# Optimization experiments

Measured on AMD Instinct MI355X. Metric: run time of the kernel, lower is better.

The kernel has to match this reference:

```python
import jax, jax.numpy as jnp
import numpy as np

B, N, C = 8, 4096, 1024
H, D = 16, 64
FF = 4096
EPS_ATTN = 1e-6
EPS_LN = 1e-5


def layer_norm(x, g, b, eps=EPS_LN):
    mu = jnp.mean(x, axis=-1, keepdims=True)
    var = jnp.mean(jnp.square(x - mu), axis=-1, keepdims=True)
    return (x - mu) * jax.lax.rsqrt(var + eps) * g + b


def phi(x):
    # elu(x) + 1
    return jnp.where(x > 0, x + 1.0, jnp.exp(x))


def setup_inputs() -> dict:
    key = jax.random.key(0)
    ks = jax.random.split(key, 8)
    src = jax.random.normal(ks[0], (B, N, C), dtype=jnp.float32)
    lengths = jax.random.randint(ks[1], (B,), int(0.75 * N), N + 1)
    src_key_padding_mask = jnp.arange(N)[None, :] >= lengths[:, None]
    s = 0.02
    qkv_w = jax.random.normal(ks[2], (3 * C, C), dtype=jnp.float32) * s
    qkv_b = jnp.zeros((3 * C,), jnp.float32)
    out_w = jax.random.normal(ks[3], (C, C), dtype=jnp.float32) * s
    out_b = jnp.zeros((C,), jnp.float32)
    w1 = jax.random.normal(ks[4], (FF, C), dtype=jnp.float32) * s
    b1 = jnp.zeros((FF,), jnp.float32)
    w2 = jax.random.normal(ks[5], (C, FF), dtype=jnp.float32) * s
    b2 = jnp.zeros((C,), jnp.float32)
    ln1_g = jnp.ones((C,), jnp.float32)
    ln1_b = jnp.zeros((C,), jnp.float32)
    ln2_g = jnp.ones((C,), jnp.float32)
    ln2_b = jnp.zeros((C,), jnp.float32)
    return dict(src=src, src_key_padding_mask=src_key_padding_mask,
                qkv_w=qkv_w, qkv_b=qkv_b, out_w=out_w, out_b=out_b,
                w1=w1, b1=b1, w2=w2, b2=b2,
                ln1_g=ln1_g, ln1_b=ln1_b, ln2_g=ln2_g, ln2_b=ln2_b)


def linear_attention(x, mask, qkv_w, qkv_b, out_w, out_b):
    b, n, c = x.shape
    qkv = (x @ qkv_w.T + qkv_b).reshape(b, n, 3, H, D)
    qkv = jnp.transpose(qkv, (2, 0, 3, 1, 4))  # [3,B,H,N,D]
    q, k, v = qkv[0], qkv[1], qkv[2]
    qf, kf = phi(q), phi(k)
    valid = (~mask).astype(kf.dtype)[:, None, :, None]  # [B,1,N,1]
    kf = kf * valid
    v = v * valid
    kv = jnp.einsum('bhnd,bhne->bhde', kf, v)          # [B,H,D,D]
    z = kf.sum(axis=2)                                  # [B,H,D]
    y_num = jnp.einsum('bhnd,bhde->bhne', qf, kv)       # [B,H,N,D]
    y_den = jnp.maximum(jnp.einsum('bhnd,bhd->bhn', qf, z), EPS_ATTN)
    y = y_num / y_den[..., None]
    y = jnp.transpose(y, (0, 2, 1, 3)).reshape(b, n, c)
    return y @ out_w.T + out_b


def reference(src, src_key_padding_mask, qkv_w, qkv_b, out_w, out_b,
              w1, b1, w2, b2, ln1_g, ln1_b, ln2_g, ln2_b):
    # pre-norm: attention block
    attn_out = linear_attention(layer_norm(src, ln1_g, ln1_b), src_key_padding_mask,
                                qkv_w, qkv_b, out_w, out_b)
    x = src + attn_out
    # pre-norm: FFN block (exact gelu, matching torch F.gelu default)
    h = jax.nn.gelu(layer_norm(x, ln2_g, ln2_b) @ w1.T + b1, approximate=False)
    return x + (h @ w2.T + b2)
```

## Files before the change

### kernel.cpp

```cpp
#include <hip/hip_runtime.h>
#include <cmath>
#include <cstdint>

#define MTOK 32768
#define CDIM 1024
#define SEQ  4096
#define NHEAD 16
#define HDIM 64
#define FFDIM 4096

typedef __attribute__((ext_vector_type(8))) short short8;
typedef __attribute__((ext_vector_type(4))) float f32x4;

static __device__ __forceinline__ float b2f(unsigned short u){
  union { unsigned int i; float f; } c; c.i = ((unsigned int)u)<<16; return c.f;
}
static __device__ __forceinline__ unsigned short f2b(float f){
  union { float f; unsigned int i; } c; c.f = f;
  return (unsigned short)((c.i + 0x7fffu + ((c.i>>16)&1u)) >> 16);
}
static __device__ __forceinline__ void async16(const void* g, void* l){
  __builtin_amdgcn_global_load_lds((const __attribute__((address_space(1))) void*)g,
                                   (__attribute__((address_space(3))) void*)l, 16, 0, 0);
}

__global__ void detect_mask_kernel(const unsigned int* __restrict__ m, int* __restrict__ flag){
  __shared__ int any;
  if(threadIdx.x==0) any=0;
  __syncthreads();
  int loc=0;
  for(int i=threadIdx.x;i<8192;i+=256) if(m[i]>1u) loc=1;
  if(loc) atomicOr(&any,1);
  __syncthreads();
  if(threadIdx.x==0) *flag=any;
}
__global__ void decode_mask_kernel(const void* __restrict__ m, const int* __restrict__ flag,
                                   float* __restrict__ validf){
  int i = blockIdx.x*256 + threadIdx.x;
  int pad = (*flag) ? (int)((const unsigned char*)m)[i] : ((const int*)m)[i];
  validf[i] = pad ? 0.f : 1.f;
}

__global__ void cast_bf16_kernel(const float* __restrict__ x, unsigned short* __restrict__ y, int n){
  int i = (blockIdx.x*256 + threadIdx.x)*4;
  if(i>=n) return;
  float4 v = *(const float4*)(x+i);
  ushort4 o; o.x=f2b(v.x); o.y=f2b(v.y); o.z=f2b(v.z); o.w=f2b(v.w);
  *(ushort4*)(y+i)=o;
}

__global__ __launch_bounds__(256) void ln_kernel(const float* __restrict__ x,
    const float* __restrict__ g, const float* __restrict__ bt, unsigned short* __restrict__ out){
  int row = blockIdx.x, t = threadIdx.x;
  const float* xr = x + (size_t)row*CDIM;
  float4 v = *(const float4*)(xr + t*4);
  float s1 = v.x+v.y+v.z+v.w;
  float s2 = v.x*v.x+v.y*v.y+v.z*v.z+v.w*v.w;
  #pragma unroll
  for(int off=32; off>0; off>>=1){ s1+=__shfl_down(s1,off); s2+=__shfl_down(s2,off); }
  __shared__ float a1[4], a2[4];
  __shared__ float mu_s, rs_s;
  if((t&63)==0){ a1[t>>6]=s1; a2[t>>6]=s2; }
  __syncthreads();
  if(t==0){
    float u1=a1[0]+a1[1]+a1[2]+a1[3], u2=a2[0]+a2[1]+a2[2]+a2[3];
    float mu=u1*(1.f/CDIM);
    mu_s=mu; rs_s=rsqrtf(u2*(1.f/CDIM)-mu*mu+1e-5f);
  }
  __syncthreads();
  float mu=mu_s, rs=rs_s;
  float4 gg=*(const float4*)(g+t*4), bb=*(const float4*)(bt+t*4);
  ushort4 o;
  o.x=f2b((v.x-mu)*rs*gg.x+bb.x);
  o.y=f2b((v.y-mu)*rs*gg.y+bb.y);
  o.z=f2b((v.z-mu)*rs*gg.z+bb.z);
  o.w=f2b((v.w-mu)*rs*gg.w+bb.w);
  *(ushort4*)(out+(size_t)row*CDIM+t*4)=o;
}

template<int MODE>
__global__ __launch_bounds__(512,2) void gemm_bt(
    const unsigned short* __restrict__ A, const unsigned short* __restrict__ Bw,
    const float* __restrict__ bias, const float* __restrict__ extra,
    float* __restrict__ Cf, unsigned short* __restrict__ Cb,
    int M, int N, int K)
{
  __shared__ __align__(16) unsigned short As[2*2*128*64];
  __shared__ __align__(16) unsigned short Bs[2*2*128*64];
  const int tid  = threadIdx.x;
  const int lane = tid & 63, wave = tid >> 6;
  const int wm = wave >> 2, wn = wave & 3;
  const int gx  = gridDim.x;
  const int f   = blockIdx.y * gx + blockIdx.x;
  const int xcd = f & 7, kk = f >> 3;
  const int nx  = kk % gx;
  const int ny  = (kk / gx) * 8 + xcd;
  const int m0 = ny*256, n0 = nx*256;
  const int r8  = lane >> 3;
  const int gch = ((lane & 7) ^ r8) * 8;
  const int l15 = lane & 15;
  const int kc  = lane >> 4, x7 = lane & 7;
  const int ch0 = ( kc      ^ x7) * 8;
  const int ch1 = ((kc + 4) ^ x7) * 8;
  const int NT  = K >> 6;

  f32x4 acc[2][2][4][2];
  #pragma unroll
  for(int a0=0;a0<2;a0++)
    #pragma unroll
    for(int a1=0;a1<2;a1++)
      #pragma unroll
      for(int a2=0;a2<4;a2++)
        #pragma unroll
        for(int a3=0;a3<2;a3++) acc[a0][a1][a2][a3]=(f32x4)(0.f);

  auto stageA = [&](int h, int bb, int kcol){
    const unsigned short* g = A + (size_t)(m0 + h*128 + wave*8 + r8)*K + kcol + gch;
    unsigned short* l = &As[((bb*2 + h)*128 + wave*8)*64];
    async16(g, l);
    async16(g + (size_t)64*K, l + 64*64);
  };
  auto stageB = [&](int h, int bb, int kcol){
    const unsigned short* g = Bw + (size_t)(n0 + h*128 + wave*8 + r8)*K + kcol + gch;
    unsigned short* l = &Bs[((bb*2 + h)*128 + wave*8)*64];
    async16(g, l);
    async16(g + (size_t)64*K, l + 64*64);
  };

  #define READ_A(H,BB) { const unsigned short* Ab=&As[((BB)*2+(H))*128*64];         \
    _Pragma("unroll") for(int fi=0;fi<4;fi++){ int ro=(wm*64+fi*16+l15)*64;          \
      af[fi][0]=*(const short8*)&Ab[ro+ch0];                                         \
      af[fi][1]=*(const short8*)&Ab[ro+ch1]; } }
  #define READ_B(H,BB,DST) { const unsigned short* Bb=&Bs[((BB)*2+(H))*128*64];      \
    _Pragma("unroll") for(int ni=0;ni<2;ni++){ int ro=(wn*32+ni*16+l15)*64;          \
      DST[ni][0]=*(const short8*)&Bb[ro+ch0];                                        \
      DST[ni][1]=*(const short8*)&Bb[ro+ch1]; } }
  #define QUAD(MQ,NQ,BV) {                                                           \
    _Pragma("unroll") for(int fi=0;fi<4;fi++)                                        \
      _Pragma("unroll") for(int ni=0;ni<2;ni++){                                     \
        acc[MQ][NQ][fi][ni]=__builtin_amdgcn_mfma_f32_16x16x32_bf16(                 \
            af[fi][0],BV[ni][0],acc[MQ][NQ][fi][ni],0,0,0);                          \
        acc[MQ][NQ][fi][ni]=__builtin_amdgcn_mfma_f32_16x16x32_bf16(                 \
            af[fi][1],BV[ni][1],acc[MQ][NQ][fi][ni],0,0,0); } }

  stageA(0,0,0); stageA(1,0,0); stageB(0,0,0); stageB(1,0,0);
  if(NT>1){
    stageA(0,1,64); stageB(0,1,64);
    asm volatile("s_waitcnt vmcnt(4)" ::: "memory");
  } else {
    asm volatile("s_waitcnt vmcnt(0)" ::: "memory");
  }
  __builtin_amdgcn_s_barrier();

  for(int t=0; t<NT; ++t){
    const int bi = t & 1, bo = (t+1) & 1;
    const int k1 = (t+1) << 6, k2 = (t+2) << 6;
    short8 af[4][2], b0v[2][2], b1v[2][2];

    READ_A(0,bi); READ_B(0,bi,b0v);
    if(t+1<NT) stageA(1,bo,k1);
    __builtin_amdgcn_s_barrier();
    asm volatile("s_waitcnt lgkmcnt(0)" ::: "memory");
    __builtin_amdgcn_s_setprio(1); QUAD(0,0,b0v); __builtin_amdgcn_s_setprio(0);
    __builtin_amdgcn_s_barrier();

    READ_B(1,bi,b1v);
    if(t+1<NT) stageB(1,bo,k1);
    __builtin_amdgcn_s_barrier();
    asm volatile("s_waitcnt lgkmcnt(0)" ::: "memory");
    __builtin_amdgcn_s_setprio(1); QUAD(0,1,b1v); __builtin_amdgcn_s_setprio(0);
    __builtin_amdgcn_s_barrier();

    READ_A(1,bi);
    if(t+2<NT) stageA(0,bi,k2);
    __builtin_amdgcn_s_barrier();
    asm volatile("s_waitcnt lgkmcnt(0)" ::: "memory");
    __builtin_amdgcn_s_setprio(1); QUAD(1,0,b0v); __builtin_amdgcn_s_setprio(0);
    __builtin_amdgcn_s_barrier();

    if(t+2<NT) stageB(0,bi,k2);
    __builtin_amdgcn_s_barrier();
    asm volatile("s_waitcnt lgkmcnt(0)" ::: "memory");
    __builtin_amdgcn_s_setprio(1); QUAD(1,1,b1v); __builtin_amdgcn_s_setprio(0);
    if(t+2<NT){ asm volatile("s_waitcnt vmcnt(4)" ::: "memory"); }
    else      { asm volatile("s_waitcnt vmcnt(0)" ::: "memory"); }
    __builtin_amdgcn_s_barrier();
  }
  #undef READ_A
  #undef READ_B
  #undef QUAD

  const int rb0 = (lane>>4)*4;
  #pragma unroll
  for(int mq=0;mq<2;mq++){
    #pragma unroll
    for(int fi=0;fi<4;fi++){
      #pragma unroll
      for(int i=0;i<4;i++){
        int m = m0 + mq*128 + wm*64 + fi*16 + rb0 + i;
        float valid = (MODE==0) ? extra[m] : 0.f;
        #pragma unroll
        for(int nq=0;nq<2;nq++){
          #pragma unroll
          for(int ni=0;ni<2;ni++){
            int n = n0 + nq*128 + wn*32 + ni*16 + l15;
            float v = acc[mq][nq][fi][ni][i] + bias[n];
            if(MODE==0){
              int part = n>>10;
              float p = (v>0.f)? (v+1.f) : __expf(v);
              float r = (part==0)? p : (part==1? p*valid : v*valid);
              Cb[(size_t)m*N + n] = f2b(r);
            } else if(MODE==1){
              size_t off=(size_t)m*N+n;
              Cf[off] = v + extra[off];
            } else if(MODE==2){
              float gl = 0.5f*v*(1.f+erff(v*0.70710678118654752f));
              Cb[(size_t)m*N+n] = f2b(gl);
            } else {
              size_t off=(size_t)m*N+n;
              Cf[off] += v;
            }
          }
        }
      }
    }
  }
}

__global__ __launch_bounds__(256) void kvz_partial_kernel(
    const unsigned short* __restrict__ qkv, float* __restrict__ kvp, float* __restrict__ zp)
{
  const int chunk = blockIdx.x;
  const int bh = blockIdx.y;
  const int b = bh>>4, h = bh&15;
  const int t = threadIdx.x;
  __shared__ float kfs[16][64];
  __shared__ float vs[16][64];
  float acc[4][4]={{0}}; float zacc[4]={0};
  const int td=t&15, te=t>>4;
  const int d0=td*4, e0=te*4;
  const int lr=t>>4, lc=(t&15)*4;
  for(int s=0;s<16;s++){
    size_t m  = (size_t)(b*SEQ + chunk*256 + s*16 + lr);
    size_t rb = m*3072 + (size_t)h*64;
    ushort4 k4 = *(const ushort4*)(qkv + rb + 1024 + lc);
    ushort4 v4 = *(const ushort4*)(qkv + rb + 2048 + lc);
    __syncthreads();
    kfs[lr][lc]=b2f(k4.x); kfs[lr][lc+1]=b2f(k4.y); kfs[lr][lc+2]=b2f(k4.z); kfs[lr][lc+3]=b2f(k4.w);
    vs [lr][lc]=b2f(v4.x); vs [lr][lc+1]=b2f(v4.y); vs [lr][lc+2]=b2f(v4.z); vs [lr][lc+3]=b2f(v4.w);
    __syncthreads();
    #pragma unroll
    for(int n=0;n<16;n++){
      float4 kq=*(const float4*)&kfs[n][d0];
      float4 vv=*(const float4*)&vs[n][e0];
      float kqa[4]={kq.x,kq.y,kq.z,kq.w};
      float vva[4]={vv.x,vv.y,vv.z,vv.w};
      #pragma unroll
      for(int i=0;i<4;i++)
        #pragma unroll
        for(int j=0;j<4;j++) acc[i][j]+=kqa[i]*vva[j];
      if(te==0){ zacc[0]+=kq.x; zacc[1]+=kq.y; zacc[2]+=kq.z; zacc[3]+=kq.w; }
    }
  }
  const int pidx = bh*16 + chunk;
  float* kvd = kvp + (size_t)pidx*4096;
  #pragma unroll
  for(int i=0;i<4;i++){
    float4 o={acc[i][0],acc[i][1],acc[i][2],acc[i][3]};
    *(float4*)(kvd + (d0+i)*64 + e0)=o;
  }
  if(te==0){
    float4 o={zacc[0],zacc[1],zacc[2],zacc[3]};
    *(float4*)(zp + (size_t)pidx*64 + d0)=o;
  }
}

__global__ void kvz_reduce_kernel(const float* __restrict__ kvp, const float* __restrict__ zp,
                                  float* __restrict__ kv, float* __restrict__ z){
  int bh = blockIdx.x, t = threadIdx.x;
  for(int j=t; j<4096; j+=256){
    float s=0;
    for(int c=0;c<16;c++) s += kvp[((size_t)bh*16+c)*4096 + j];
    kv[(size_t)bh*4096 + j] = s;
  }
  if(t<64){
    float s=0;
    for(int c=0;c<16;c++) s += zp[((size_t)bh*16+c)*64 + t];
    z[bh*64+t]=s;
  }
}

__global__ __launch_bounds__(256) void y_kernel(
    const unsigned short* __restrict__ qkv, const float* __restrict__ kv,
    const float* __restrict__ z, unsigned short* __restrict__ ybuf)
{
  const int nch = blockIdx.x;
  const int bh  = blockIdx.y;
  const int b = bh>>4, h = bh&15;
  const int t = threadIdx.x;
  __shared__ float kvs[64][64];
  __shared__ float qfs[64][68];
  __shared__ float zs[64];
  for(int j=t*4; j<4096; j+=1024){
    float4 vv=*(const float4*)(kv+(size_t)bh*4096+j);
    ((float*)kvs)[j]=vv.x; ((float*)kvs)[j+1]=vv.y; ((float*)kvs)[j+2]=vv.z; ((float*)kvs)[j+3]=vv.w;
  }
  if(t<64) zs[t]=z[bh*64+t];
  for(int s=0;s<4;s++){
    int row=s*16+(t>>4), col=(t&15)*4;
    size_t m=(size_t)(b*SEQ+nch*64+row);
    ushort4 q4=*(const ushort4*)(qkv+m*3072+(size_t)h*64+col);
    qfs[row][col]=b2f(q4.x); qfs[row][col+1]=b2f(q4.y); qfs[row][col+2]=b2f(q4.z); qfs[row][col+3]=b2f(q4.w);
  }
  __syncthreads();
  const int tn=t>>4, te=t&15;
  const int nr0=tn*4, e0=te*4;
  float acc[4][4]={{0}}; float den[4]={0};
  #pragma unroll 4
  for(int d=0;d<64;d++){
    float4 kv4=*(const float4*)&kvs[d][e0];
    float zd=zs[d];
    #pragma unroll
    for(int i=0;i<4;i++){
      float q=qfs[nr0+i][d];
      acc[i][0]+=q*kv4.x; acc[i][1]+=q*kv4.y; acc[i][2]+=q*kv4.z; acc[i][3]+=q*kv4.w;
      den[i]+=q*zd;
    }
  }
  #pragma unroll
  for(int i=0;i<4;i++){
    float inv=1.f/fmaxf(den[i],1e-6f);
    ushort4 o;
    o.x=f2b(acc[i][0]*inv); o.y=f2b(acc[i][1]*inv); o.z=f2b(acc[i][2]*inv); o.w=f2b(acc[i][3]*inv);
    size_t m=(size_t)(b*SEQ+nch*64+nr0+i);
    *(ushort4*)(ybuf+m*1024+(size_t)h*64+e0)=o;
  }
}

extern "C" void kernel_launch(void* const* d_in, const int* in_sizes, int n_in,
                              void* d_out, int out_size, void* d_ws, size_t ws_size,
                              hipStream_t stream)
{
  const float* src   = (const float*)d_in[0];
  const void*  mask  = d_in[1];
  const float* qkv_w = (const float*)d_in[2];
  const float* qkv_b = (const float*)d_in[3];
  const float* out_w = (const float*)d_in[4];
  const float* out_b = (const float*)d_in[5];
  const float* w1    = (const float*)d_in[6];
  const float* b1    = (const float*)d_in[7];
  const float* w2    = (const float*)d_in[8];
  const float* b2    = (const float*)d_in[9];
  const float* ln1g  = (const float*)d_in[10];
  const float* ln1b  = (const float*)d_in[11];
  const float* ln2g  = (const float*)d_in[12];
  const float* ln2b  = (const float*)d_in[13];
  float* out = (float*)d_out;
  char* ws = (char*)d_ws;

  size_t o = 0;
  int* flag = (int*)(ws);                         o += 256;
  float* validf = (float*)(ws+o);                 o += (size_t)MTOK*4;
  unsigned short* wqb = (unsigned short*)(ws+o);  o += (size_t)3072*1024*2;
  unsigned short* wob = (unsigned short*)(ws+o);  o += (size_t)1024*1024*2;
  unsigned short* w1b = (unsigned short*)(ws+o);  o += (size_t)4096*1024*2;
  unsigned short* w2b = (unsigned short*)(ws+o);  o += (size_t)1024*4096*2;
  unsigned short* bufA = (unsigned short*)(ws+o); o += (size_t)MTOK*1024*2;
  char* R = ws+o;                                 o += (size_t)MTOK*4096*2;
  unsigned short* qkvbuf = (unsigned short*)R;
  float* kvp = (float*)(R + (size_t)MTOK*3072*2);
  float* zp  = (float*)(R + (size_t)MTOK*3072*2 + (size_t)2048*4096*4);
  unsigned short* hbuf = (unsigned short*)R;
  float* kv = (float*)(ws+o);                     o += (size_t)128*4096*4;
  float* zv = (float*)(ws+o);                     o += (size_t)128*64*4;

  detect_mask_kernel<<<1,256,0,stream>>>((const unsigned int*)mask, flag);
  decode_mask_kernel<<<MTOK/256,256,0,stream>>>(mask, flag, validf);
  cast_bf16_kernel<<<3072,256,0,stream>>>(qkv_w, wqb, 3072*1024);
  cast_bf16_kernel<<<1024,256,0,stream>>>(out_w, wob, 1024*1024);
  cast_bf16_kernel<<<4096,256,0,stream>>>(w1,  w1b, 4096*1024);
  cast_bf16_kernel<<<8192,256,0,stream>>>(w2,  w2b, 1024*4096);

  ln_kernel<<<MTOK,256,0,stream>>>(src, ln1g, ln1b, bufA);
  gemm_bt<0><<<dim3(3072/256, MTOK/256),512,0,stream>>>(bufA, wqb, qkv_b, validf, nullptr, qkvbuf, MTOK,3072,1024);
  kvz_partial_kernel<<<dim3(16,128),256,0,stream>>>(qkvbuf, kvp, zp);
  kvz_reduce_kernel<<<128,256,0,stream>>>(kvp, zp, kv, zv);
  y_kernel<<<dim3(64,128),256,0,stream>>>(qkvbuf, kv, zv, bufA);
  gemm_bt<1><<<dim3(1024/256, MTOK/256),512,0,stream>>>(bufA, wob, out_b, src, out, nullptr, MTOK,1024,1024);
  ln_kernel<<<MTOK,256,0,stream>>>(out, ln2g, ln2b, bufA);
  gemm_bt<2><<<dim3(4096/256, MTOK/256),512,0,stream>>>(bufA, w1b, b1, nullptr, nullptr, hbuf, MTOK,4096,1024);
  gemm_bt<3><<<dim3(1024/256, MTOK/256),512,0,stream>>>(hbuf, w2b, b2, nullptr, out, nullptr, MTOK,1024,4096);
}
```

Baseline: 1.561 ms.

## Template GEMM on K and reorder async LDS staging for deeper prefetch

Makes the K dimension a template parameter so address arithmetic and trip counts are compile-time constants, and precomputes per-thread global base pointers. Reorders the async global-to-LDS staging so three tiles are in flight at the prologue and next-tile loads are issued earlier within each iteration, with vmcnt waits raised to match. It also relaxes the lgkmcnt waits and adds a sched_barrier, aiming to hide global load latency behind MFMA work. The buffer reuse ordering changes, which risks races if the waits and barriers don't exactly cover overwritten LDS regions.

```diff
diff --git a/kernel.cpp b/kernel.cpp
--- a/kernel.cpp
+++ b/kernel.cpp
@@ -78,12 +78,12 @@
   *(ushort4*)(out+(size_t)row*CDIM+t*4)=o;
 }
 
-template<int MODE>
+template<int MODE, int KDIM>
 __global__ __launch_bounds__(512,2) void gemm_bt(
     const unsigned short* __restrict__ A, const unsigned short* __restrict__ Bw,
     const float* __restrict__ bias, const float* __restrict__ extra,
     float* __restrict__ Cf, unsigned short* __restrict__ Cb,
-    int M, int N, int K)
+    int M, int N)
 {
   __shared__ __align__(16) unsigned short As[2*2*128*64];
   __shared__ __align__(16) unsigned short Bs[2*2*128*64];
@@ -98,11 +98,13 @@
   const int m0 = ny*256, n0 = nx*256;
   const int r8  = lane >> 3;
   const int gch = ((lane & 7) ^ r8) * 8;
+  const unsigned short* gA = A  + (size_t)(m0 + wave*8 + r8)*KDIM + gch;
+  const unsigned short* gB = Bw + (size_t)(n0 + wave*8 + r8)*KDIM + gch;
   const int l15 = lane & 15;
   const int kc  = lane >> 4, x7 = lane & 7;
   const int ch0 = ( kc      ^ x7) * 8;
   const int ch1 = ((kc + 4) ^ x7) * 8;
-  const int NT  = K >> 6;
+  const int NT  = KDIM >> 6;
 
   f32x4 acc[2][2][4][2];
   #pragma unroll
@@ -114,17 +116,17 @@
         #pragma unroll
         for(int a3=0;a3<2;a3++) acc[a0][a1][a2][a3]=(f32x4)(0.f);
 
-  auto stageA = [&](int h, int bb, int kcol){
-    const unsigned short* g = A + (size_t)(m0 + h*128 + wave*8 + r8)*K + kcol + gch;
+  auto stA = [&](int h, int bb, int kcol){
+    const unsigned short* g = gA + (size_t)h*128*KDIM + kcol;
     unsigned short* l = &As[((bb*2 + h)*128 + wave*8)*64];
     async16(g, l);
-    async16(g + (size_t)64*K, l + 64*64);
+    async16(g + (size_t)64*KDIM, l + 4096);
   };
-  auto stageB = [&](int h, int bb, int kcol){
-    const unsigned short* g = Bw + (size_t)(n0 + h*128 + wave*8 + r8)*K + kcol + gch;
+  auto stB = [&](int h, int bb, int kcol){
+    const unsigned short* g = gB + (size_t)h*128*KDIM + kcol;
     unsigned short* l = &Bs[((bb*2 + h)*128 + wave*8)*64];
     async16(g, l);
-    async16(g + (size_t)64*K, l + 64*64);
+    async16(g + (size_t)64*KDIM, l + 4096);
   };
 
   #define READ_A(H,BB) { const unsigned short* Ab=&As[((BB)*2+(H))*128*64];         \
@@ -143,47 +145,48 @@
         acc[MQ][NQ][fi][ni]=__builtin_amdgcn_mfma_f32_16x16x32_bf16(                 \
             af[fi][1],BV[ni][1],acc[MQ][NQ][fi][ni],0,0,0); } }
 
-  stageA(0,0,0); stageA(1,0,0); stageB(0,0,0); stageB(1,0,0);
+  stA(0,0,0); stB(0,0,0); stB(1,0,0); stA(1,0,0);
   if(NT>1){
-    stageA(0,1,64); stageB(0,1,64);
-    asm volatile("s_waitcnt vmcnt(4)" ::: "memory");
+    stA(0,1,64); stB(0,1,64); stA(1,1,64);
+    asm volatile("s_waitcnt vmcnt(6)" ::: "memory");
   } else {
     asm volatile("s_waitcnt vmcnt(0)" ::: "memory");
   }
   __builtin_amdgcn_s_barrier();
 
   for(int t=0; t<NT; ++t){
-    const int bi = t & 1, bo = (t+1) & 1;
+    const int bi = t & 1, bo = bi ^ 1;
     const int k1 = (t+1) << 6, k2 = (t+2) << 6;
     short8 af[4][2], b0v[2][2], b1v[2][2];
 
     READ_A(0,bi); READ_B(0,bi,b0v);
-    if(t+1<NT) stageA(1,bo,k1);
-    __builtin_amdgcn_s_barrier();
-    asm volatile("s_waitcnt lgkmcnt(0)" ::: "memory");
+    if(t+1<NT) stB(1,bo,k1);
+    asm volatile("s_waitcnt lgkmcnt(8)");
+    __builtin_amdgcn_s_barrier();
+    asm volatile("s_waitcnt lgkmcnt(0)");
     __builtin_amdgcn_s_setprio(1); QUAD(0,0,b0v); __builtin_amdgcn_s_setprio(0);
     __builtin_amdgcn_s_barrier();
 
     READ_B(1,bi,b1v);
-    if(t+1<NT) stageB(1,bo,k1);
-    __builtin_amdgcn_s_barrier();
-    asm volatile("s_waitcnt lgkmcnt(0)" ::: "memory");
+    if(t+2<NT) stA(0,bi,k2);
+    __builtin_amdgcn_s_barrier();
+    asm volatile("s_waitcnt lgkmcnt(0)");
     __builtin_amdgcn_s_setprio(1); QUAD(0,1,b1v); __builtin_amdgcn_s_setprio(0);
     __builtin_amdgcn_s_barrier();
 
     READ_A(1,bi);
-    if(t+2<NT) stageA(0,bi,k2);
-    __builtin_amdgcn_s_barrier();
-    asm volatile("s_waitcnt lgkmcnt(0)" ::: "memory");
+    if(t+2<NT) stB(0,bi,k2);
+    __builtin_amdgcn_s_barrier();
+    asm volatile("s_waitcnt lgkmcnt(0)");
     __builtin_amdgcn_s_setprio(1); QUAD(1,0,b0v); __builtin_amdgcn_s_setprio(0);
     __builtin_amdgcn_s_barrier();
 
-    if(t+2<NT) stageB(0,bi,k2);
-    __builtin_amdgcn_s_barrier();
-    asm volatile("s_waitcnt lgkmcnt(0)" ::: "memory");
+    if(t+2<NT) stA(1,bi,k2);
+    __builtin_amdgcn_s_barrier();
     __builtin_amdgcn_s_setprio(1); QUAD(1,1,b1v); __builtin_amdgcn_s_setprio(0);
-    if(t+2<NT){ asm volatile("s_waitcnt vmcnt(4)" ::: "memory"); }
+    if(t+2<NT){ asm volatile("s_waitcnt vmcnt(6)" ::: "memory"); }
     else      { asm volatile("s_waitcnt vmcnt(0)" ::: "memory"); }
+    __builtin_amdgcn_sched_barrier(0);
     __builtin_amdgcn_s_barrier();
   }
   #undef READ_A
@@ -382,12 +385,12 @@
   cast_bf16_kernel<<<8192,256,0,stream>>>(w2,  w2b, 1024*4096);
 
   ln_kernel<<<MTOK,256,0,stream>>>(src, ln1g, ln1b, bufA);
-  gemm_bt<0><<<dim3(3072/256, MTOK/256),512,0,stream>>>(bufA, wqb, qkv_b, validf, nullptr, qkvbuf, MTOK,3072,1024);
+  gemm_bt<0,1024><<<dim3(3072/256, MTOK/256),512,0,stream>>>(bufA, wqb, qkv_b, validf, nullptr, qkvbuf, MTOK,3072);
   kvz_partial_kernel<<<dim3(16,128),256,0,stream>>>(qkvbuf, kvp, zp);
   kvz_reduce_kernel<<<128,256,0,stream>>>(kvp, zp, kv, zv);
   y_kernel<<<dim3(64,128),256,0,stream>>>(qkvbuf, kv, zv, bufA);
-  gemm_bt<1><<<dim3(1024/256, MTOK/256),512,0,stream>>>(bufA, wob, out_b, src, out, nullptr, MTOK,1024,1024);
+  gemm_bt<1,1024><<<dim3(1024/256, MTOK/256),512,0,stream>>>(bufA, wob, out_b, src, out, nullptr, MTOK,1024);
   ln_kernel<<<MTOK,256,0,stream>>>(out, ln2g, ln2b, bufA);
-  gemm_bt<2><<<dim3(4096/256, MTOK/256),512,0,stream>>>(bufA, w1b, b1, nullptr, nullptr, hbuf, MTOK,4096,1024);
-  gemm_bt<3><<<dim3(1024/256, MTOK/256),512,0,stream>>>(hbuf, w2b, b2, nullptr, out, nullptr, MTOK,1024,4096);
-}
+  gemm_bt<2,1024><<<dim3(4096/256, MTOK/256),512,0,stream>>>(bufA, w1b, b1, nullptr, nullptr, hbuf, MTOK,4096);
+  gemm_bt<3,4096><<<dim3(1024/256, MTOK/256),512,0,stream>>>(hbuf, w2b, b2, nullptr, out, nullptr, MTOK,1024);
+}
```

After: 1.488 ms. -4.6%, faster.
